# Kernel optimization log

Measured on AMD Instinct MI355X. Metric: run time of the kernel, lower is better.

The kernel has to match this reference:

```python
import jax, jax.numpy as jnp
import numpy as np

B, C, H, W = 8, 256, 48, 48
CK = 64  # C // k
WSCALE = 0.3 / np.sqrt(C)  # keep exp(QK^T) finite (original has no 1/sqrt(d) scaling)


def conv1x1(x, w, b):
    # x: (B,C,H,W), w: (O,C,1,1), b: (O,) -> (B,O,H,W)
    return jnp.einsum('bchw,oc->bohw', x, w[:, :, 0, 0]) + b[None, :, None, None]


def setup_inputs() -> dict:
    key = jax.random.key(0)
    ks = jax.random.split(key, 6)
    x = jax.random.normal(ks[0], (B, C, H, W), dtype=jnp.float32)
    qw = jax.random.normal(ks[1], (CK, C, 1, 1), dtype=jnp.float32) * WSCALE
    kw = jax.random.normal(ks[2], (CK, C, 1, 1), dtype=jnp.float32) * WSCALE
    vw = jax.random.normal(ks[3], (C, C, 1, 1), dtype=jnp.float32) * (1.0 / np.sqrt(C))
    gw = jax.random.normal(ks[4], (C, C, 1, 1), dtype=jnp.float32) * (1.0 / np.sqrt(C))
    zk = jnp.zeros((CK,), dtype=jnp.float32)
    zc = jnp.zeros((C,), dtype=jnp.float32)
    return {
        'x': x,
        'query_weight': qw, 'query_bias': zk,
        'key_weight': kw, 'key_bias': zk,
        'value_weight': vw, 'value_bias': zc,
        'gamma_weight': gw, 'gamma_bias': zc,
        'k': 4,
    }


def reference(x, query_weight, query_bias, key_weight, key_bias,
              value_weight, value_bias, gamma_weight, gamma_bias, k):
    b, c, h, w = x.shape
    n = h * w
    q = conv1x1(x, query_weight, query_bias).reshape(b, -1, n)   # (B,Ck,N)
    kk = conv1x1(x, key_weight, key_bias).reshape(b, -1, n)      # (B,Ck,N)
    # energy[b,i,j] = q_i . k_j  (queries on rows, no sqrt(d) scaling)
    energy = jnp.einsum('bci,bcj->bij', q, kk)                   # (B,N,N)
    energy = jnp.exp(energy)
    energy = energy / jnp.sum(energy, axis=2, keepdims=True)     # unnormalized-softmax over keys
    v = conv1x1(x, value_weight, value_bias).reshape(b, c, n)    # (B,C,N)
    # out[b,c,j] = sum_i v[b,c,i] * energy[b,i,j]  (faithful to torch.bmm(V, energy))
    out = jnp.einsum('bci,bij->bcj', v, energy).reshape(b, c, h, w)
    out = conv1x1(out, gamma_weight, gamma_bias)
    return out
```

## Files before the change

### kernel.cpp

```cpp
#include <hip/hip_runtime.h>

#define BATCH 8
#define CIN   256
#define NPIX  2304
#define CKD   64
#define NIT   (NPIX / 16)
#define NIC   (NPIX / 32)
#define NJB   (NPIX / 64)
#define NQ    4
#define ICQ   (NIC / NQ)
#define IT16Q (NIT / NQ)

typedef _Float16 f16;
typedef __attribute__((ext_vector_type(4))) _Float16 f16x4;
typedef __attribute__((ext_vector_type(8))) _Float16 f16x8;
typedef __attribute__((ext_vector_type(4))) float    f32x4;


__global__ __launch_bounds__(256) void cast_w(
    const float* __restrict__ qw, const float* __restrict__ kw,
    const float* __restrict__ vw, const float* __restrict__ gw,
    f16* __restrict__ Wqk, f16* __restrict__ Wv, f16* __restrict__ Wg)
{
    int idx = (blockIdx.x * 256 + threadIdx.x) * 4;
    const float* src;
    f16* dst;
    if (idx < 16384)      { src = qw + idx;           dst = Wqk + idx; }
    else if (idx < 32768) { src = kw + (idx - 16384); dst = Wqk + idx; }
    else if (idx < 98304) { src = vw + (idx - 32768); dst = Wv + (idx - 32768); }
    else                  { src = gw + (idx - 98304); dst = Wg + (idx - 98304); }
    float4 v = *(const float4*)src;
    f16x4 h = { (f16)v.x, (f16)v.y, (f16)v.z, (f16)v.w };
    *(f16x4*)dst = h;
}

__global__ __launch_bounds__(256) void cast_xT(
    const float* __restrict__ x, f16* __restrict__ xT)
{
    __shared__ float s[64][65];
    const int t = threadIdx.x;
    const int n0 = blockIdx.x * 64, c0 = blockIdx.y * 64, b = blockIdx.z;
    const float* xb = x + ((size_t)b * CIN + c0) * NPIX + n0;

    const int cl = t >> 4, ng = (t & 15) * 4;
    #pragma unroll
    for (int p = 0; p < 4; ++p) {
        float4 v = *(const float4*)(xb + (size_t)(cl + 16 * p) * NPIX + ng);
        s[cl + 16 * p][ng + 0] = v.x;
        s[cl + 16 * p][ng + 1] = v.y;
        s[cl + 16 * p][ng + 2] = v.z;
        s[cl + 16 * p][ng + 3] = v.w;
    }
    __syncthreads();
    const int nl = t >> 2, cs = (t & 3) * 16;
    f16 h[16];
    #pragma unroll
    for (int j = 0; j < 16; ++j) h[j] = (f16)s[cs + j][nl];
    f16* gp = &xT[((size_t)b * NPIX + n0 + nl) * CIN + c0 + cs];
    *(f16x8*)gp       = *(f16x8*)&h[0];
    *(f16x8*)(gp + 8) = *(f16x8*)&h[8];
}

__global__ __launch_bounds__(256) void qk_conv_mfma(
    const f16* __restrict__ xT, const f16* __restrict__ Wqk,
    const float* __restrict__ qbias, const float* __restrict__ kbias,
    f16* __restrict__ q_blk, f16* __restrict__ k_blk)
{
    __shared__ __align__(16) f16 us[32 * 136];
    const int t = threadIdx.x, w = t >> 6, lane = t & 63;
    const int quad = lane >> 4, l16 = lane & 15;
    const int wm = w & 1, wn = w >> 1;
    const int n0 = blockIdx.x * 32, b = blockIdx.y;

    const f16* bp = xT + ((size_t)b * NPIX + n0 + 16 * wn + l16) * CIN;
    const f16* ap = Wqk + (size_t)(64 * wm + l16) * CIN;

    f32x4 acc[4];
    #pragma unroll
    for (int mt = 0; mt < 4; ++mt) acc[mt] = (f32x4){0.f, 0.f, 0.f, 0.f};

    #pragma unroll
    for (int kk = 0; kk < CIN; kk += 32) {
        f16x8 bf = *(const f16x8*)(bp + kk + quad * 8);
        #pragma unroll
        for (int mt = 0; mt < 4; ++mt) {
            f16x8 af = *(const f16x8*)(ap + (size_t)mt * 16 * CIN + kk + quad * 8);
            acc[mt] = __builtin_amdgcn_mfma_f32_16x16x32_f16(af, bf, acc[mt], 0, 0, 0);
        }
    }
    const float* bias = wm ? kbias - 64 : qbias;
    #pragma unroll
    for (int mt = 0; mt < 4; ++mt) {
        int ob = 64 * wm + 16 * mt + quad * 4;
        #pragma unroll
        for (int r = 0; r < 4; ++r)
            us[(16 * wn + l16) * 136 + ob + r] = (f16)(acc[mt][r] + bias[ob + r]);
    }
    __syncthreads();
    {
        int ks2 = t >> 7, nt = (t >> 6) & 1, ln = t & 63;
        const f16* usr = &us[(nt * 16 + (ln & 15)) * 136 + ks2 * 32 + (ln >> 4) * 8];
        size_t base = (((size_t)b * NIT + (n0 >> 4) + nt) * 2 + ks2) * 512 + ln * 8;
        *(f16x8*)&q_blk[base] = *(const f16x8*)(usr);
        *(f16x8*)&k_blk[base] = *(const f16x8*)(usr + 64);
    }
}

#define ESL 136
__global__ __launch_bounds__(256) void energy_S(
    const f16* __restrict__ q_blk, const f16* __restrict__ k_blk,
    float* __restrict__ Pred)
{
    __shared__ __align__(16) f16 es[64 * ESL];
    __shared__ float red2[2][128];
    const int t    = threadIdx.x;
    const int w    = t >> 6, lane = t & 63;
    const int quad = lane >> 4, l16 = lane & 15;
    const int j0 = blockIdx.x * 64, i0 = blockIdx.y * 128, b = blockIdx.z;
    const size_t ln8 = (size_t)lane * 8;
    const f16* qb = q_blk + (size_t)b * NIT * 2 * 512 + ln8;

    f32x4 acc[8];
    #pragma unroll
    for (int mt = 0; mt < 8; ++mt) acc[mt] = (f32x4){0.f, 0.f, 0.f, 0.f};

    #pragma unroll
    for (int ks = 0; ks < 2; ++ks) {
        f16x8 bf = *(const f16x8*)(k_blk +
            (((size_t)b * NIT + (j0 >> 4) + w) * 2 + ks) * 512 + ln8);
        #pragma unroll
        for (int mt = 0; mt < 8; ++mt) {
            f16x8 af = *(const f16x8*)(qb + ((size_t)((i0 >> 4) + mt) * 2 + ks) * 512);
            acc[mt] = __builtin_amdgcn_mfma_f32_16x16x32_f16(af, bf, acc[mt], 0, 0, 0);
        }
    }

    #pragma unroll
    for (int mt = 0; mt < 8; ++mt) {
        f16x4 h = { (f16)__expf(acc[mt][0]), (f16)__expf(acc[mt][1]),
                    (f16)__expf(acc[mt][2]), (f16)__expf(acc[mt][3]) };
        *(f16x4*)&es[(16 * w + l16) * ESL + 16 * mt + quad * 4] = h;
    }
    __syncthreads();
    {
        int i = t & 127, jq = t >> 7;
        float s = 0.f;
        #pragma unroll
        for (int jj = 0; jj < 32; ++jj)
            s += (float)es[(jq * 32 + jj) * ESL + i];
        red2[jq][i] = s;
    }
    __syncthreads();
    if (t < 128)
        Pred[((size_t)blockIdx.x * BATCH + b) * NPIX + i0 + t] =
            red2[0][t] + red2[1][t];
}

__global__ __launch_bounds__(256) void reduce_S(
    const float* __restrict__ Pred, float* __restrict__ S)
{
    const size_t BN = (size_t)BATCH * NPIX;
    size_t idx = (size_t)blockIdx.x * 256 + threadIdx.x;
    float s = 0.f;
    #pragma unroll
    for (int jb = 0; jb < NJB; ++jb)
        s += Pred[(size_t)jb * BN + idx];
    S[idx] = s;
}

__global__ __launch_bounds__(256) void v_conv_mfma(
    const f16* __restrict__ xT, const f16* __restrict__ Wv,
    const float* __restrict__ vbias, const float* __restrict__ S,
    f16* __restrict__ u_blk)
{
    __shared__ __align__(16) f16 smem[9216];
    f16* As = smem;
    f16* Bs = smem + 128 * 40;
    f16* us = smem;
    const int t = threadIdx.x, w = t >> 6, lane = t & 63;
    const int quad = lane >> 4, l16 = lane & 15;
    const int wm = w & 1, wn = w >> 1;
    const int i0 = blockIdx.x * 64, c0 = blockIdx.y * 128, b = blockIdx.z;
    const int sub = t >> 2, le = t & 3;
    const f16* srcA = Wv + (size_t)(c0 + sub) * CIN + le * 8;
    const f16* srcB = xT + ((size_t)b * NPIX + i0 + sub) * CIN + le * 8;
    const int ldsw = sub * 40 + le * 8;

    f32x4 acc[4][2];
    #pragma unroll
    for (int mt = 0; mt < 4; ++mt)
        #pragma unroll
        for (int nt = 0; nt < 2; ++nt)
            acc[mt][nt] = (f32x4){0.f, 0.f, 0.f, 0.f};

    for (int kk = 0; kk < CIN; kk += 32) {
        f16x8 ta0 = *(const f16x8*)(srcA + kk);
        f16x8 ta1 = *(const f16x8*)(srcA + (size_t)64 * CIN + kk);
        f16x8 tb0 = *(const f16x8*)(srcB + kk);
        __syncthreads();
        *(f16x8*)&As[ldsw]           = ta0;
        *(f16x8*)&As[64 * 40 + ldsw] = ta1;
        *(f16x8*)&Bs[ldsw]           = tb0;
        __syncthreads();
        f16x8 af[4], bf[2];
        #pragma unroll
        for (int mt = 0; mt < 4; ++mt)
            af[mt] = *(const f16x8*)&As[(64 * wm + 16 * mt + l16) * 40 + quad * 8];
        #pragma unroll
        for (int nt = 0; nt < 2; ++nt)
            bf[nt] = *(const f16x8*)&Bs[(32 * wn + 16 * nt + l16) * 40 + quad * 8];
        #pragma unroll
        for (int mt = 0; mt < 4; ++mt)
            #pragma unroll
            for (int nt = 0; nt < 2; ++nt)
                acc[mt][nt] = __builtin_amdgcn_mfma_f32_16x16x32_f16(
                    af[mt], bf[nt], acc[mt][nt], 0, 0, 0);
    }

    __syncthreads();
    #pragma unroll
    for (int nt = 0; nt < 2; ++nt) {
        int i = 32 * wn + 16 * nt + l16;
        float is = 1.0f / S[(size_t)b * NPIX + i0 + i];
        #pragma unroll
        for (int mt = 0; mt < 4; ++mt)
            #pragma unroll
            for (int r = 0; r < 4; ++r) {
                int c = 64 * wm + 16 * mt + quad * 4 + r;
                us[c * 72 + i] = (f16)((acc[mt][nt][r] + vbias[c0 + c]) * is);
            }
    }
    __syncthreads();
    #pragma unroll
    for (int p = 0; p < 4; ++p) {
        int g  = t + 256 * p;
        int ct = g >> 7, ic = (g >> 6) & 1, ln = g & 63;
        f16x8 v = *(const f16x8*)&us[(ct * 16 + (ln & 15)) * 72 + ic * 32 + (ln >> 4) * 8];
        *(f16x8*)&u_blk[(((size_t)b * 16 + (c0 >> 4) + ct) * NIC + (i0 >> 5) + ic) * 512 + ln * 8] = v;
    }
}

__global__ __launch_bounds__(512, 4) void fused_bmm(
    const f16* __restrict__ q_blk, const f16* __restrict__ k_blk,
    const f16* __restrict__ u_blk,
    f16* __restrict__ o1A, f16* __restrict__ o1B,
    f16* __restrict__ o1C, f16* __restrict__ o1D)
{
    extern __shared__ __align__(16) f16 es[];
    const int t = threadIdx.x, w = t >> 6, lane = t & 63;
    const int quad = lane >> 4, l16 = lane & 15;
    const int bid = blockIdx.x;
    const int b   = bid & 7;
    const int r   = bid >> 3;
    const int q   = r & 3;
    const int jb  = r >> 2;
    const int j0  = jb * 64;
    f16* __restrict__ o1h = (q == 0) ? o1A : (q == 1) ? o1B : (q == 2) ? o1C : o1D;
    const size_t ln8 = (size_t)lane * 8;

    const f16* qb = q_blk + (size_t)b * NIT * 2 * 512 + ln8;
    const f16* ub = u_blk + (size_t)b * 16 * NIC * 512 + ln8;

    const int iw0 = w >> 1;
    const int jh  = w & 1;

    f16x8 kf[2][2];
    #pragma unroll
    for (int jj = 0; jj < 2; ++jj)
        #pragma unroll
        for (int ks = 0; ks < 2; ++ks)
            kf[jj][ks] = *(const f16x8*)(k_blk +
                (((size_t)b * NIT + (j0 >> 4) + jh + 2 * jj) * 2 + ks) * 512 + ln8);

    const int CT0 = w * 2;
    const int woff = (quad >> 1) * 128 + l16 * 8 + (quad & 1) * 4;

    f32x4 acc[2][4];
    #pragma unroll
    for (int mt = 0; mt < 2; ++mt)
        #pragma unroll
        for (int jt = 0; jt < 4; ++jt)
            acc[mt][jt] = (f32x4){0.f, 0.f, 0.f, 0.f};

#define ULD(ct, icg) (*(const f16x8*)(ub + ((size_t)(CT0 + (ct)) * NIC + (icg)) * 512))

    #pragma unroll 1
    for (int gen = 0; gen < 2; ++gen) {
        const int t0 = gen * 18;
        for (int i16 = t0 + iw0; i16 < t0 + 18; i16 += 4) {
            const int gi = q * IT16Q + i16;
            f16x8 q0 = *(const f16x8*)(qb + ((size_t)gi * 2 + 0) * 512);
            f16x8 q1 = *(const f16x8*)(qb + ((size_t)gi * 2 + 1) * 512);
            f32x4 e0 = (f32x4){0.f, 0.f, 0.f, 0.f};
            f32x4 e1 = (f32x4){0.f, 0.f, 0.f, 0.f};
            e0 = __builtin_amdgcn_mfma_f32_16x16x32_f16(q0, kf[0][0], e0, 0, 0, 0);
            e0 = __builtin_amdgcn_mfma_f32_16x16x32_f16(q1, kf[0][1], e0, 0, 0, 0);
            e1 = __builtin_amdgcn_mfma_f32_16x16x32_f16(q0, kf[1][0], e1, 0, 0, 0);
            e1 = __builtin_amdgcn_mfma_f32_16x16x32_f16(q1, kf[1][1], e1, 0, 0, 0);
            f16x4 h0 = { (f16)__expf(e0[0]), (f16)__expf(e0[1]),
                         (f16)__expf(e0[2]), (f16)__expf(e0[3]) };
            f16x4 h1 = { (f16)__expf(e1[0]), (f16)__expf(e1[1]),
                         (f16)__expf(e1[2]), (f16)__expf(e1[3]) };
            const int il  = i16 - t0;
            const int wo2 = ((il & 1) * 2) * 128 + woff;
            const int tb  = (il >> 1) * 4;
            *(f16x4*)&es[(size_t)(tb + jh) * 512 + wo2]     = h0;
            *(f16x4*)&es[(size_t)(tb + jh + 2) * 512 + wo2] = h1;
        }

        const int g0 = q * ICQ + gen * 9;
        f16x8 ua = ULD(0, g0),     ub2 = ULD(1, g0);
        f16x8 na = ULD(0, g0 + 1), nb  = ULD(1, g0 + 1);
        asm volatile("s_waitcnt lgkmcnt(0)" ::: "memory");
        __builtin_amdgcn_s_barrier();

        __builtin_amdgcn_s_setprio(1);
        for (int ic2 = 0; ic2 < 9; ++ic2) {
            f16x8 fa, fb2;
            if (ic2 + 2 < 9) { fa = ULD(0, g0 + ic2 + 2); fb2 = ULD(1, g0 + ic2 + 2); }
            #pragma unroll
            for (int jt = 0; jt < 4; ++jt) {
                f16x8 bf = *(const f16x8*)&es[(size_t)(ic2 * 4 + jt) * 512 + ln8];
                acc[0][jt] = __builtin_amdgcn_mfma_f32_16x16x32_f16(ua,  bf, acc[0][jt], 0, 0, 0);
                acc[1][jt] = __builtin_amdgcn_mfma_f32_16x16x32_f16(ub2, bf, acc[1][jt], 0, 0, 0);
            }
            ua = na; ub2 = nb; na = fa; nb = fb2;
        }
        __builtin_amdgcn_s_setprio(0);
        __builtin_amdgcn_s_barrier();
    }
#undef ULD

    #pragma unroll
    for (int mt = 0; mt < 2; ++mt) {
        int cb = 32 * w + 16 * mt + quad * 4;
        #pragma unroll
        for (int jt = 0; jt < 4; ++jt) {
            int j = j0 + 16 * jt + l16;
            f16x4 h2 = { (f16)acc[mt][jt][0], (f16)acc[mt][jt][1],
                         (f16)acc[mt][jt][2], (f16)acc[mt][jt][3] };
            *(f16x4*)&o1h[((size_t)b * NPIX + j) * CIN + cb] = h2;
        }
    }
}

__global__ __launch_bounds__(256) void gamma_conv_mfma(
    const f16* __restrict__ o1A, const f16* __restrict__ o1B,
    const f16* __restrict__ o1C, const f16* __restrict__ o1D,
    const f16* __restrict__ Wg,
    const float* __restrict__ gbias, float* __restrict__ out)
{
    __shared__ __align__(16) f16 As[128 * 40];
    __shared__ __align__(16) f16 Bs[64 * 40];
    const int t = threadIdx.x, w = t >> 6, lane = t & 63;
    const int quad = lane >> 4, l16 = lane & 15;
    const int wm = w & 1, wn = w >> 1;
    const int j0 = blockIdx.x * 64, o0 = blockIdx.y * 128, b = blockIdx.z;
    const int sub = t >> 2, le = t & 3;
    const f16* srcA  = Wg + (size_t)(o0 + sub) * CIN + le * 8;
    const size_t boff = ((size_t)b * NPIX + j0 + sub) * CIN + le * 8;
    const int ldsw = sub * 40 + le * 8;

    f32x4 acc[4][2];
    #pragma unroll
    for (int mt = 0; mt < 4; ++mt)
        #pragma unroll
        for (int nt = 0; nt < 2; ++nt)
            acc[mt][nt] = (f32x4){0.f, 0.f, 0.f, 0.f};

    for (int kk = 0; kk < CIN; kk += 32) {
        f16x8 ta0 = *(const f16x8*)(srcA + kk);
        f16x8 ta1 = *(const f16x8*)(srcA + (size_t)64 * CIN + kk);
        f16x8 t0 = *(const f16x8*)(o1A + boff + kk);
        f16x8 t1 = *(const f16x8*)(o1B + boff + kk);
        f16x8 t2 = *(const f16x8*)(o1C + boff + kk);
        f16x8 t3 = *(const f16x8*)(o1D + boff + kk);
        f16x8 tb0;
        #pragma unroll
        for (int e = 0; e < 8; ++e)
            tb0[e] = (f16)(((float)t0[e] + (float)t1[e]) +
                           ((float)t2[e] + (float)t3[e]));
        __syncthreads();
        *(f16x8*)&As[ldsw]           = ta0;
        *(f16x8*)&As[64 * 40 + ldsw] = ta1;
        *(f16x8*)&Bs[ldsw]           = tb0;
        __syncthreads();
        f16x8 af[4], bf[2];
        #pragma unroll
        for (int mt = 0; mt < 4; ++mt)
            af[mt] = *(const f16x8*)&As[(64 * wm + 16 * mt + l16) * 40 + quad * 8];
        #pragma unroll
        for (int nt = 0; nt < 2; ++nt)
            bf[nt] = *(const f16x8*)&Bs[(32 * wn + 16 * nt + l16) * 40 + quad * 8];
        #pragma unroll
        for (int mt = 0; mt < 4; ++mt)
            #pragma unroll
            for (int nt = 0; nt < 2; ++nt)
                acc[mt][nt] = __builtin_amdgcn_mfma_f32_16x16x32_f16(
                    af[mt], bf[nt], acc[mt][nt], 0, 0, 0);
    }

    #pragma unroll
    for (int mt = 0; mt < 4; ++mt)
        #pragma unroll
        for (int r = 0; r < 4; ++r) {
            int o = o0 + 64 * wm + 16 * mt + quad * 4 + r;
            float bv = gbias[o];
            #pragma unroll
            for (int nt = 0; nt < 2; ++nt) {
                int j = j0 + 32 * wn + 16 * nt + l16;
                out[((size_t)b * CIN + o) * NPIX + j] = acc[mt][nt][r] + bv;
            }
        }
}

extern "C" void kernel_launch(void* const* d_in, const int* in_sizes, int n_in,
                              void* d_out, int out_size, void* d_ws, size_t ws_size,
                              hipStream_t stream) {
    const float* x   = (const float*)d_in[0];
    const float* qw  = (const float*)d_in[1];
    const float* qbv = (const float*)d_in[2];
    const float* kw  = (const float*)d_in[3];
    const float* kbv = (const float*)d_in[4];
    const float* vw  = (const float*)d_in[5];
    const float* vbv = (const float*)d_in[6];
    const float* gw  = (const float*)d_in[7];
    const float* gbv = (const float*)d_in[8];
    float* out = (float*)d_out;

    const size_t BCN  = (size_t)BATCH * CIN * NPIX;
    const size_t BN   = (size_t)BATCH * NPIX;
    const size_t BNCK = (size_t)BATCH * NPIX * CKD;

    f16* q_blk = (f16*)d_ws;
    f16* k_blk = q_blk + BNCK;
    f16* u_blk = k_blk + BNCK;
    f16* xT    = u_blk + BCN;
    f16* o1T   = xT + BCN;
    f16* Wqk   = o1T + BCN;
    f16* Wv    = Wqk + 128 * 256;
    f16* Wg    = Wv + 256 * 256;
    float* S   = (float*)(Wg + 256 * 256);
    float* Pred= S + BN;
    f16* o1C   = (f16*)(Pred + (size_t)NJB * BN);
    f16* o1D   = o1C + BCN;

    cast_w<<<160, 256, 0, stream>>>(qw, kw, vw, gw, Wqk, Wv, Wg);
    cast_xT<<<dim3(NPIX / 64, CIN / 64, BATCH), 256, 0, stream>>>(x, xT);
    qk_conv_mfma<<<dim3(NPIX / 32, BATCH), 256, 0, stream>>>(xT, Wqk, qbv, kbv, q_blk, k_blk);
    energy_S<<<dim3(NPIX / 64, NPIX / 128, BATCH), 256, 0, stream>>>(q_blk, k_blk, Pred);
    reduce_S<<<(int)(BN / 256), 256, 0, stream>>>(Pred, S);
    v_conv_mfma<<<dim3(NPIX / 64, CIN / 128, BATCH), 256, 0, stream>>>(xT, Wv, vbv, S, u_blk);
    fused_bmm<<<NJB * NQ * BATCH, 512, 36 * 1024, stream>>>(
        q_blk, k_blk, u_blk, o1T, xT, o1C, o1D);
    gamma_conv_mfma<<<dim3(NPIX / 64, CIN / 128, BATCH), 256, 0, stream>>>(
        o1T, xT, o1C, o1D, Wg, gbv, out);
}
```

Before: 198.7 us.

## Halve fused_bmm block to 4 waves with 64-channel tiles per wave

```diff
diff --git a/kernel.cpp b/kernel.cpp
--- a/kernel.cpp
+++ b/kernel.cpp
@@ -240,7 +240,7 @@
     }
 }
 
-__global__ __launch_bounds__(512, 4) void fused_bmm(
+__global__ __launch_bounds__(256, 3) void fused_bmm(
     const f16* __restrict__ q_blk, const f16* __restrict__ k_blk,
     const f16* __restrict__ u_blk,
     f16* __restrict__ o1A, f16* __restrict__ o1B,
@@ -261,23 +261,18 @@
     const f16* qb = q_blk + (size_t)b * NIT * 2 * 512 + ln8;
     const f16* ub = u_blk + (size_t)b * 16 * NIC * 512 + ln8;
 
-    const int iw0 = w >> 1;
-    const int jh  = w & 1;
-
-    f16x8 kf[2][2];
-    #pragma unroll
-    for (int jj = 0; jj < 2; ++jj)
-        #pragma unroll
-        for (int ks = 0; ks < 2; ++ks)
-            kf[jj][ks] = *(const f16x8*)(k_blk +
-                (((size_t)b * NIT + (j0 >> 4) + jh + 2 * jj) * 2 + ks) * 512 + ln8);
-
-    const int CT0 = w * 2;
+    f16x8 kf[2];
+    #pragma unroll
+    for (int ks = 0; ks < 2; ++ks)
+        kf[ks] = *(const f16x8*)(k_blk +
+            (((size_t)b * NIT + (j0 >> 4) + w) * 2 + ks) * 512 + ln8);
+
+    const int CT0 = w * 4;
     const int woff = (quad >> 1) * 128 + l16 * 8 + (quad & 1) * 4;
 
-    f32x4 acc[2][4];
-    #pragma unroll
-    for (int mt = 0; mt < 2; ++mt)
+    f32x4 acc[4][4];
+    #pragma unroll
+    for (int mt = 0; mt < 4; ++mt)
         #pragma unroll
         for (int jt = 0; jt < 4; ++jt)
             acc[mt][jt] = (f32x4){0.f, 0.f, 0.f, 0.f};
@@ -287,44 +282,47 @@
     #pragma unroll 1
     for (int gen = 0; gen < 2; ++gen) {
         const int t0 = gen * 18;
-        for (int i16 = t0 + iw0; i16 < t0 + 18; i16 += 4) {
-            const int gi = q * IT16Q + i16;
+        #pragma unroll 2
+        for (int il = 0; il < 18; ++il) {
+            const int gi = q * IT16Q + t0 + il;
             f16x8 q0 = *(const f16x8*)(qb + ((size_t)gi * 2 + 0) * 512);
             f16x8 q1 = *(const f16x8*)(qb + ((size_t)gi * 2 + 1) * 512);
             f32x4 e0 = (f32x4){0.f, 0.f, 0.f, 0.f};
-            f32x4 e1 = (f32x4){0.f, 0.f, 0.f, 0.f};
-            e0 = __builtin_amdgcn_mfma_f32_16x16x32_f16(q0, kf[0][0], e0, 0, 0, 0);
-            e0 = __builtin_amdgcn_mfma_f32_16x16x32_f16(q1, kf[0][1], e0, 0, 0, 0);
-            e1 = __builtin_amdgcn_mfma_f32_16x16x32_f16(q0, kf[1][0], e1, 0, 0, 0);
-            e1 = __builtin_amdgcn_mfma_f32_16x16x32_f16(q1, kf[1][1], e1, 0, 0, 0);
+            e0 = __builtin_amdgcn_mfma_f32_16x16x32_f16(q0, kf[0], e0, 0, 0, 0);
+            e0 = __builtin_amdgcn_mfma_f32_16x16x32_f16(q1, kf[1], e0, 0, 0, 0);
             f16x4 h0 = { (f16)__expf(e0[0]), (f16)__expf(e0[1]),
                          (f16)__expf(e0[2]), (f16)__expf(e0[3]) };
-            f16x4 h1 = { (f16)__expf(e1[0]), (f16)__expf(e1[1]),
-                         (f16)__expf(e1[2]), (f16)__expf(e1[3]) };
-            const int il  = i16 - t0;
             const int wo2 = ((il & 1) * 2) * 128 + woff;
             const int tb  = (il >> 1) * 4;
-            *(f16x4*)&es[(size_t)(tb + jh) * 512 + wo2]     = h0;
-            *(f16x4*)&es[(size_t)(tb + jh + 2) * 512 + wo2] = h1;
+            *(f16x4*)&es[(size_t)(tb + w) * 512 + wo2] = h0;
         }
 
         const int g0 = q * ICQ + gen * 9;
-        f16x8 ua = ULD(0, g0),     ub2 = ULD(1, g0);
-        f16x8 na = ULD(0, g0 + 1), nb  = ULD(1, g0 + 1);
+        f16x8 ua[4], na[4];
+        #pragma unroll
+        for (int ct = 0; ct < 4; ++ct) ua[ct] = ULD(ct, g0);
+        #pragma unroll
+        for (int ct = 0; ct < 4; ++ct) na[ct] = ULD(ct, g0 + 1);
         asm volatile("s_waitcnt lgkmcnt(0)" ::: "memory");
         __builtin_amdgcn_s_barrier();
 
         __builtin_amdgcn_s_setprio(1);
         for (int ic2 = 0; ic2 < 9; ++ic2) {
-            f16x8 fa, fb2;
-            if (ic2 + 2 < 9) { fa = ULD(0, g0 + ic2 + 2); fb2 = ULD(1, g0 + ic2 + 2); }
+            f16x8 fa[4];
+            if (ic2 + 2 < 9) {
+                #pragma unroll
+                for (int ct = 0; ct < 4; ++ct) fa[ct] = ULD(ct, g0 + ic2 + 2);
+            }
             #pragma unroll
             for (int jt = 0; jt < 4; ++jt) {
                 f16x8 bf = *(const f16x8*)&es[(size_t)(ic2 * 4 + jt) * 512 + ln8];
-                acc[0][jt] = __builtin_amdgcn_mfma_f32_16x16x32_f16(ua,  bf, acc[0][jt], 0, 0, 0);
-                acc[1][jt] = __builtin_amdgcn_mfma_f32_16x16x32_f16(ub2, bf, acc[1][jt], 0, 0, 0);
+                #pragma unroll
+                for (int mt = 0; mt < 4; ++mt)
+                    acc[mt][jt] = __builtin_amdgcn_mfma_f32_16x16x32_f16(
+                        ua[mt], bf, acc[mt][jt], 0, 0, 0);
             }
-            ua = na; ub2 = nb; na = fa; nb = fb2;
+            #pragma unroll
+            for (int ct = 0; ct < 4; ++ct) { ua[ct] = na[ct]; na[ct] = fa[ct]; }
         }
         __builtin_amdgcn_s_setprio(0);
         __builtin_amdgcn_s_barrier();
@@ -332,8 +330,8 @@
 #undef ULD
 
     #pragma unroll
-    for (int mt = 0; mt < 2; ++mt) {
-        int cb = 32 * w + 16 * mt + quad * 4;
+    for (int mt = 0; mt < 4; ++mt) {
+        int cb = 64 * w + 16 * mt + quad * 4;
         #pragma unroll
         for (int jt = 0; jt < 4; ++jt) {
             int j = j0 + 16 * jt + l16;
@@ -451,7 +449,7 @@
     energy_S<<<dim3(NPIX / 64, NPIX / 128, BATCH), 256, 0, stream>>>(q_blk, k_blk, Pred);
     reduce_S<<<(int)(BN / 256), 256, 0, stream>>>(Pred, S);
     v_conv_mfma<<<dim3(NPIX / 64, CIN / 128, BATCH), 256, 0, stream>>>(xT, Wv, vbv, S, u_blk);
-    fused_bmm<<<NJB * NQ * BATCH, 512, 36 * 1024, stream>>>(
+    fused_bmm<<<NJB * NQ * BATCH, 256, 36 * 1024, stream>>>(
         q_blk, k_blk, u_blk, o1T, xT, o1C, o1D);
     gamma_conv_mfma<<<dim3(NPIX / 64, CIN / 128, BATCH), 256, 0, stream>>>(
         o1T, xT, o1C, o1D, Wg, gbv, out);
```

New measurement: 203.1 us. +2.2%, slower.

## Fold gamma conv into value weights and drop split-K reduction stage

Applied to the files above, without the earlier changes.

```diff
diff --git a/kernel.cpp b/kernel.cpp
--- a/kernel.cpp
+++ b/kernel.cpp
@@ -7,9 +7,6 @@
 #define NIT   (NPIX / 16)
 #define NIC   (NPIX / 32)
 #define NJB   (NPIX / 64)
-#define NQ    4
-#define ICQ   (NIC / NQ)
-#define IT16Q (NIT / NQ)
 
 typedef _Float16 f16;
 typedef __attribute__((ext_vector_type(4))) _Float16 f16x4;
@@ -19,19 +16,30 @@
 
 __global__ __launch_bounds__(256) void cast_w(
     const float* __restrict__ qw, const float* __restrict__ kw,
-    const float* __restrict__ vw, const float* __restrict__ gw,
-    f16* __restrict__ Wqk, f16* __restrict__ Wv, f16* __restrict__ Wg)
+    f16* __restrict__ Wqk)
 {
     int idx = (blockIdx.x * 256 + threadIdx.x) * 4;
-    const float* src;
-    f16* dst;
-    if (idx < 16384)      { src = qw + idx;           dst = Wqk + idx; }
-    else if (idx < 32768) { src = kw + (idx - 16384); dst = Wqk + idx; }
-    else if (idx < 98304) { src = vw + (idx - 32768); dst = Wv + (idx - 32768); }
-    else                  { src = gw + (idx - 98304); dst = Wg + (idx - 98304); }
+    const float* src = (idx < 16384) ? qw + idx : kw + (idx - 16384);
     float4 v = *(const float4*)src;
     f16x4 h = { (f16)v.x, (f16)v.y, (f16)v.z, (f16)v.w };
-    *(f16x4*)dst = h;
+    *(f16x4*)&Wqk[idx] = h;
+}
+
+__global__ __launch_bounds__(256) void make_wgv(
+    const float* __restrict__ gw, const float* __restrict__ vw,
+    const float* __restrict__ vb,
+    f16* __restrict__ Wgv, float* __restrict__ b2)
+{
+    const int o = blockIdx.x, c2 = threadIdx.x;
+    float s = 0.f;
+    for (int c = 0; c < CIN; ++c)
+        s += gw[o * CIN + c] * vw[(size_t)c * CIN + c2];
+    Wgv[(size_t)o * CIN + c2] = (f16)s;
+    if (c2 == 0) {
+        float sb = 0.f;
+        for (int c = 0; c < CIN; ++c) sb += gw[o * CIN + c] * vb[c];
+        b2[o] = sb;
+    }
 }
 
 __global__ __launch_bounds__(256) void cast_xT(
@@ -242,20 +250,16 @@
 
 __global__ __launch_bounds__(512, 4) void fused_bmm(
     const f16* __restrict__ q_blk, const f16* __restrict__ k_blk,
-    const f16* __restrict__ u_blk,
-    f16* __restrict__ o1A, f16* __restrict__ o1B,
-    f16* __restrict__ o1C, f16* __restrict__ o1D)
+    const f16* __restrict__ u_blk, const float* __restrict__ gbias,
+    float* __restrict__ out)
 {
     extern __shared__ __align__(16) f16 es[];
     const int t = threadIdx.x, w = t >> 6, lane = t & 63;
     const int quad = lane >> 4, l16 = lane & 15;
     const int bid = blockIdx.x;
     const int b   = bid & 7;
-    const int r   = bid >> 3;
-    const int q   = r & 3;
-    const int jb  = r >> 2;
+    const int jb  = bid >> 3;
     const int j0  = jb * 64;
-    f16* __restrict__ o1h = (q == 0) ? o1A : (q == 1) ? o1B : (q == 2) ? o1C : o1D;
     const size_t ln8 = (size_t)lane * 8;
 
     const f16* qb = q_blk + (size_t)b * NIT * 2 * 512 + ln8;
@@ -285,10 +289,10 @@
 #define ULD(ct, icg) (*(const f16x8*)(ub + ((size_t)(CT0 + (ct)) * NIC + (icg)) * 512))
 
     #pragma unroll 1
-    for (int gen = 0; gen < 2; ++gen) {
+    for (int gen = 0; gen < 8; ++gen) {
         const int t0 = gen * 18;
-        for (int i16 = t0 + iw0; i16 < t0 + 18; i16 += 4) {
-            const int gi = q * IT16Q + i16;
+        for (int il = iw0; il < 18; il += 4) {
+            const int gi = t0 + il;
             f16x8 q0 = *(const f16x8*)(qb + ((size_t)gi * 2 + 0) * 512);
             f16x8 q1 = *(const f16x8*)(qb + ((size_t)gi * 2 + 1) * 512);
             f32x4 e0 = (f32x4){0.f, 0.f, 0.f, 0.f};
@@ -301,14 +305,13 @@
                          (f16)__expf(e0[2]), (f16)__expf(e0[3]) };
             f16x4 h1 = { (f16)__expf(e1[0]), (f16)__expf(e1[1]),
                          (f16)__expf(e1[2]), (f16)__expf(e1[3]) };
-            const int il  = i16 - t0;
             const int wo2 = ((il & 1) * 2) * 128 + woff;
             const int tb  = (il >> 1) * 4;
             *(f16x4*)&es[(size_t)(tb + jh) * 512 + wo2]     = h0;
             *(f16x4*)&es[(size_t)(tb + jh + 2) * 512 + wo2] = h1;
         }
 
-        const int g0 = q * ICQ + gen * 9;
+        const int g0 = gen * 9;
         f16x8 ua = ULD(0, g0),     ub2 = ULD(1, g0);
         f16x8 na = ULD(0, g0 + 1), nb  = ULD(1, g0 + 1);
         asm volatile("s_waitcnt lgkmcnt(0)" ::: "memory");
@@ -337,81 +340,12 @@
         #pragma unroll
         for (int jt = 0; jt < 4; ++jt) {
             int j = j0 + 16 * jt + l16;
-            f16x4 h2 = { (f16)acc[mt][jt][0], (f16)acc[mt][jt][1],
-                         (f16)acc[mt][jt][2], (f16)acc[mt][jt][3] };
-            *(f16x4*)&o1h[((size_t)b * NPIX + j) * CIN + cb] = h2;
-        }
-    }
-}
-
-__global__ __launch_bounds__(256) void gamma_conv_mfma(
-    const f16* __restrict__ o1A, const f16* __restrict__ o1B,
-    const f16* __restrict__ o1C, const f16* __restrict__ o1D,
-    const f16* __restrict__ Wg,
-    const float* __restrict__ gbias, float* __restrict__ out)
-{
-    __shared__ __align__(16) f16 As[128 * 40];
-    __shared__ __align__(16) f16 Bs[64 * 40];
-    const int t = threadIdx.x, w = t >> 6, lane = t & 63;
-    const int quad = lane >> 4, l16 = lane & 15;
-    const int wm = w & 1, wn = w >> 1;
-    const int j0 = blockIdx.x * 64, o0 = blockIdx.y * 128, b = blockIdx.z;
-    const int sub = t >> 2, le = t & 3;
-    const f16* srcA  = Wg + (size_t)(o0 + sub) * CIN + le * 8;
-    const size_t boff = ((size_t)b * NPIX + j0 + sub) * CIN + le * 8;
-    const int ldsw = sub * 40 + le * 8;
-
-    f32x4 acc[4][2];
-    #pragma unroll
-    for (int mt = 0; mt < 4; ++mt)
-        #pragma unroll
-        for (int nt = 0; nt < 2; ++nt)
-            acc[mt][nt] = (f32x4){0.f, 0.f, 0.f, 0.f};
-
-    for (int kk = 0; kk < CIN; kk += 32) {
-        f16x8 ta0 = *(const f16x8*)(srcA + kk);
-        f16x8 ta1 = *(const f16x8*)(srcA + (size_t)64 * CIN + kk);
-        f16x8 t0 = *(const f16x8*)(o1A + boff + kk);
-        f16x8 t1 = *(const f16x8*)(o1B + boff + kk);
-        f16x8 t2 = *(const f16x8*)(o1C + boff + kk);
-        f16x8 t3 = *(const f16x8*)(o1D + boff + kk);
-        f16x8 tb0;
-        #pragma unroll
-        for (int e = 0; e < 8; ++e)
-            tb0[e] = (f16)(((float)t0[e] + (float)t1[e]) +
-                           ((float)t2[e] + (float)t3[e]));
-        __syncthreads();
-        *(f16x8*)&As[ldsw]           = ta0;
-        *(f16x8*)&As[64 * 40 + ldsw] = ta1;
-        *(f16x8*)&Bs[ldsw]           = tb0;
-        __syncthreads();
-        f16x8 af[4], bf[2];
-        #pragma unroll
-        for (int mt = 0; mt < 4; ++mt)
-            af[mt] = *(const f16x8*)&As[(64 * wm + 16 * mt + l16) * 40 + quad * 8];
-        #pragma unroll
-        for (int nt = 0; nt < 2; ++nt)
-            bf[nt] = *(const f16x8*)&Bs[(32 * wn + 16 * nt + l16) * 40 + quad * 8];
-        #pragma unroll
-        for (int mt = 0; mt < 4; ++mt)
             #pragma unroll
-            for (int nt = 0; nt < 2; ++nt)
-                acc[mt][nt] = __builtin_amdgcn_mfma_f32_16x16x32_f16(
-                    af[mt], bf[nt], acc[mt][nt], 0, 0, 0);
-    }
-
-    #pragma unroll
-    for (int mt = 0; mt < 4; ++mt)
-        #pragma unroll
-        for (int r = 0; r < 4; ++r) {
-            int o = o0 + 64 * wm + 16 * mt + quad * 4 + r;
-            float bv = gbias[o];
-            #pragma unroll
-            for (int nt = 0; nt < 2; ++nt) {
-                int j = j0 + 32 * wn + 16 * nt + l16;
-                out[((size_t)b * CIN + o) * NPIX + j] = acc[mt][nt][r] + bv;
-            }
-        }
+            for (int r = 0; r < 4; ++r)
+                out[((size_t)b * CIN + cb + r) * NPIX + j] =
+                    acc[mt][jt][r] + gbias[cb + r];
+        }
+    }
 }
 
 extern "C" void kernel_launch(void* const* d_in, const int* in_sizes, int n_in,
@@ -436,23 +370,18 @@
     f16* k_blk = q_blk + BNCK;
     f16* u_blk = k_blk + BNCK;
     f16* xT    = u_blk + BCN;
-    f16* o1T   = xT + BCN;
-    f16* Wqk   = o1T + BCN;
-    f16* Wv    = Wqk + 128 * 256;
-    f16* Wg    = Wv + 256 * 256;
-    float* S   = (float*)(Wg + 256 * 256);
-    float* Pred= S + BN;
-    f16* o1C   = (f16*)(Pred + (size_t)NJB * BN);
-    f16* o1D   = o1C + BCN;
-
-    cast_w<<<160, 256, 0, stream>>>(qw, kw, vw, gw, Wqk, Wv, Wg);
+    f16* Wqk   = xT + BCN;
+    f16* Wgv   = Wqk + 128 * 256;
+    float* S   = (float*)(Wgv + 256 * 256);
+    float* b2  = S + BN;
+    float* Pred= b2 + 256;
+
+    cast_w<<<32, 256, 0, stream>>>(qw, kw, Wqk);
+    make_wgv<<<256, 256, 0, stream>>>(gw, vw, vbv, Wgv, b2);
     cast_xT<<<dim3(NPIX / 64, CIN / 64, BATCH), 256, 0, stream>>>(x, xT);
     qk_conv_mfma<<<dim3(NPIX / 32, BATCH), 256, 0, stream>>>(xT, Wqk, qbv, kbv, q_blk, k_blk);
     energy_S<<<dim3(NPIX / 64, NPIX / 128, BATCH), 256, 0, stream>>>(q_blk, k_blk, Pred);
     reduce_S<<<(int)(BN / 256), 256, 0, stream>>>(Pred, S);
-    v_conv_mfma<<<dim3(NPIX / 64, CIN / 128, BATCH), 256, 0, stream>>>(xT, Wv, vbv, S, u_blk);
-    fused_bmm<<<NJB * NQ * BATCH, 512, 36 * 1024, stream>>>(
-        q_blk, k_blk, u_blk, o1T, xT, o1C, o1D);
-    gamma_conv_mfma<<<dim3(NPIX / 64, CIN / 128, BATCH), 256, 0, stream>>>(
-        o1T, xT, o1C, o1D, Wg, gbv, out);
-}
+    v_conv_mfma<<<dim3(NPIX / 64, CIN / 128, BATCH), 256, 0, stream>>>(xT, Wgv, b2, S, u_blk);
+    fused_bmm<<<NJB * BATCH, 512, 36 * 1024, stream>>>(q_blk, k_blk, u_blk, gbv, out);
+}
```

Result: no change. 198.1 us (-0.3%).
